# Kernel optimization log

Measured on AMD Instinct MI355X. Metric: run time of the kernel, lower is better.

The kernel has to match this reference:

```python
import jax, jax.numpy as jnp
import numpy as np

MARGIN = 0.5
SCALE = 64.0

N, D, C, S = 512, 512, 100000, 1


def setup_inputs() -> dict:
    key = jax.random.key(0)
    k1, k2, k3 = jax.random.split(key, 3)
    emb = jax.random.normal(k1, (N, D), dtype=jnp.float32)
    # Real face pipelines feed L2-normalized embeddings; also keeps acos well-conditioned.
    emb = emb / jnp.linalg.norm(emb, axis=1, keepdims=True)
    w = jax.random.normal(k2, (D, C, S), dtype=jnp.float32)
    labels = jax.random.randint(k3, (N,), 0, C)
    target = jax.nn.one_hot(labels, C, dtype=jnp.float32)  # [N, C]
    return {"embedding_batch": emb, "w_param": w, "target_batch": target}


def reference(embedding_batch, w_param, target_batch):
    # normalize class centers over the embedding dim (dim=0 of w)
    w_n = w_param / jnp.linalg.norm(w_param, axis=0, keepdims=True)  # [D, C, S]
    # cosine similarities via GEMM instead of broadcast mult-reduce: [N, C, S]
    cos = jnp.einsum('nd,dcs->ncs', embedding_batch, w_n)
    cos = jnp.clip(cos, -1.0, 1.0)
    cos = jnp.max(cos, axis=2)                    # best subclass -> [N, C]
    theta = jnp.arccos(cos)                       # [N, C]
    logits = jnp.cos(theta + target_batch * MARGIN) * SCALE
    # faithful to the original: softmax over dim=0 (the batch axis)
    return jax.nn.softmax(logits, axis=0)
```

## Files before the change

### kernel.cpp

```cpp
#include <hip/hip_runtime.h>
#include <hip/hip_bf16.h>


static constexpr int DIM    = 512;
static constexpr int NROWS  = 512;
static constexpr int NCLS   = 100000;
static constexpr int BC     = 32;
static constexpr int BK     = 32;
static constexpr int NSTEP  = DIM / BK;
static constexpr int MT     = NROWS / 16;
static constexpr int NBLK   = NCLS / BC;

static constexpr float COS_M = 0.87758256189037271611f;
static constexpr float SIN_M = 0.47942553860420300027f;
static constexpr float SCALE = 64.0f;

typedef __attribute__((ext_vector_type(8))) short bf16x8;
typedef __attribute__((ext_vector_type(4))) float f32x4;

#define SYNC_LDS()                                             \
  do {                                                         \
    asm volatile("s_waitcnt lgkmcnt(0)" ::: "memory");         \
    __builtin_amdgcn_s_barrier();                              \
    __builtin_amdgcn_sched_barrier(0);                         \
  } while (0)

__device__ __forceinline__ unsigned short f2bf(float f) {
  union { float f; unsigned u; } v; v.f = f;
  unsigned u = v.u;
  return (unsigned short)((u + 0x7FFFu + ((u >> 16) & 1u)) >> 16);
}

__global__ void prep_afrag(const float* __restrict__ emb,
                           unsigned short* __restrict__ afrag) {
  const int idx = blockIdx.x * blockDim.x + threadIdx.x;
  const int l  = idx & 63;
  const int mt = (idx >> 6) & 31;
  const int ks = idx >> 11;
  const int row = mt * 16 + (l & 15);
  const int k0  = ks * 32 + (l >> 4) * 8;

  unsigned short t[8];
#pragma unroll
  for (int j = 0; j < 8; ++j) t[j] = f2bf(emb[row * DIM + k0 + j]);

  uint4 v;
  v.x = (unsigned)t[0] | ((unsigned)t[1] << 16);
  v.y = (unsigned)t[2] | ((unsigned)t[3] << 16);
  v.z = (unsigned)t[4] | ((unsigned)t[5] << 16);
  v.w = (unsigned)t[6] | ((unsigned)t[7] << 16);
  *reinterpret_cast<uint4*>(&afrag[(size_t)idx * 8]) = v;
}

__device__ __forceinline__ float2 ldr2(const float* __restrict__ m, int r, int c) {
  return *reinterpret_cast<const float2*>(m + (size_t)r * NCLS + c);
}

__global__ __launch_bounds__(512, 4)
void arcface_fused(const float* __restrict__ w,
                   const float* __restrict__ tgt,
                   const unsigned short* __restrict__ afrag,
                   float* __restrict__ out) {
  __shared__ float S1[BK][36];
  __shared__ alignas(16) unsigned short S2[128][8];
  __shared__ float red[8][BC];
  __shared__ float colv[BC];
  __shared__ float rnS[BC];
  __shared__ unsigned char labL[NROWS];

  const int tid = threadIdx.x;
  const int wv  = tid >> 6;
  const int l   = tid & 63;
  const int lh  = l >> 4;
  const int ll  = l & 15;
  const int c0  = blockIdx.x * BC;

  const int sk  = tid >> 4;
  const int sc2 = tid & 15;
  const int scg = c0 + sc2 * 2;

  if (tid < 128) *reinterpret_cast<unsigned*>(&labL[tid * 4]) = 0u;
  __syncthreads();

  int cj[2];
#pragma unroll
  for (int j = 0; j < 2; ++j) cj[j] = c0 + j * 16 + ll;

  const unsigned short* pA[4];
#pragma unroll
  for (int i = 0; i < 4; ++i)
    pA[i] = afrag + ((size_t)(wv * 4 + i) * 64 + l) * 8;

  f32x4 acc[4][2] = {};
  float nx = 0.f, ny = 0.f;

  bf16x8 a[4], an[4];
#pragma unroll
  for (int i = 0; i < 4; ++i) {
    a[i]  = *reinterpret_cast<const bf16x8*>(pA[i]);
    an[i] = a[i];
  }
  float2 v0 = ldr2(w,   sk,      scg);
  float2 t0 = ldr2(tgt, sk,      scg);
  float2 v1 = ldr2(w,   BK + sk, scg);
  float2 t1 = ldr2(tgt, BK + sk, scg);

  for (int ks = 0; ks < NSTEP; ++ks) {
    nx += v0.x * v0.x; ny += v0.y * v0.y;
    *reinterpret_cast<float2*>(&S1[sk][sc2 * 2]) = v0;

    {
      const int row = ks * BK + sk;
      if (t0.x > 0.5f) labL[row] = (unsigned char)(sc2 * 2 + 1);
      if (t0.y > 0.5f) labL[row] = (unsigned char)(sc2 * 2 + 2);
    }
    v0 = v1; t0 = t1;

    if (ks + 1 < NSTEP) {
#pragma unroll
      for (int i = 0; i < 4; ++i)
        an[i] = *reinterpret_cast<const bf16x8*>(pA[i] + (size_t)(ks + 1) * MT * 64 * 8);
    }
    if (ks + 2 < NSTEP) {
      v1 = ldr2(w,   (ks + 2) * BK + sk, scg);
      t1 = ldr2(tgt, (ks + 2) * BK + sk, scg);
    }

    SYNC_LDS();

    if (tid < 256) {
      const int tc = tid & 31;
      const int tl = (tid >> 5) & 3;
      const int hf = (tid >> 7) & 1;
      const int kb = tl * 8 + hf * 4;
      float x0 = S1[kb + 0][tc], x1 = S1[kb + 1][tc];
      float x2 = S1[kb + 2][tc], x3 = S1[kb + 3][tc];
      uint2 pk;
      pk.x = (unsigned)f2bf(x0) | ((unsigned)f2bf(x1) << 16);
      pk.y = (unsigned)f2bf(x2) | ((unsigned)f2bf(x3) << 16);
      *reinterpret_cast<uint2*>(&S2[tl * 32 + tc][hf * 4]) = pk;
    }

    SYNC_LDS();

    bf16x8 b[2];
#pragma unroll
    for (int j = 0; j < 2; ++j)
      b[j] = *reinterpret_cast<const bf16x8*>(&S2[lh * 32 + j * 16 + ll][0]);
#pragma unroll
    for (int i = 0; i < 4; ++i)
#pragma unroll
      for (int j = 0; j < 2; ++j)
        acc[i][j] = __builtin_amdgcn_mfma_f32_16x16x32_bf16(a[i], b[j], acc[i][j], 0, 0, 0);
#pragma unroll
    for (int i = 0; i < 4; ++i) a[i] = an[i];
  }

  __syncthreads();
  *reinterpret_cast<float2*>(&S1[sk][sc2 * 2]) = make_float2(nx, ny);
  __syncthreads();
  if (tid < BC) {
    float s = 0.f;
#pragma unroll
    for (int k = 0; k < BK; ++k) s += S1[k][tid];
    rnS[tid] = rsqrtf(fmaxf(s, 1e-20f));
  }
  __syncthreads();
  float rn[2];
#pragma unroll
  for (int j = 0; j < 2; ++j) rn[j] = rnS[j * 16 + ll];

  int lab[4][4];
#pragma unroll
  for (int i = 0; i < 4; ++i)
#pragma unroll
    for (int q = 0; q < 4; ++q)
      lab[i][q] = (int)labL[wv * 64 + i * 16 + lh * 4 + q] - 1;

  float mx[2] = {-3.4e38f, -3.4e38f};
#pragma unroll
  for (int j = 0; j < 2; ++j) {
    const int jl = j * 16 + ll;
#pragma unroll
    for (int i = 0; i < 4; ++i) {
#pragma unroll
      for (int q = 0; q < 4; ++q) {
        float cosv = acc[i][j][q] * rn[j];
        cosv = fminf(fmaxf(cosv, -1.f), 1.f);
        float lg;
        if (lab[i][q] == jl) {
          const float s = sqrtf(fmaxf(1.f - cosv * cosv, 0.f));
          lg = cosv * COS_M - s * SIN_M;
        } else {
          lg = cosv;
        }
        lg *= SCALE;
        acc[i][j][q] = lg;
        mx[j] = fmaxf(mx[j], lg);
      }
    }
  }

#pragma unroll
  for (int j = 0; j < 2; ++j) {
    mx[j] = fmaxf(mx[j], __shfl_xor(mx[j], 16, 64));
    mx[j] = fmaxf(mx[j], __shfl_xor(mx[j], 32, 64));
  }
  if (l < 16) {
#pragma unroll
    for (int j = 0; j < 2; ++j) red[wv][j * 16 + l] = mx[j];
  }
  __syncthreads();
  if (tid < BC) {
    float m = red[0][tid];
#pragma unroll
    for (int v2 = 1; v2 < 8; ++v2) m = fmaxf(m, red[v2][tid]);
    colv[tid] = m;
  }
  __syncthreads();
  float cmax[2];
#pragma unroll
  for (int j = 0; j < 2; ++j) cmax[j] = colv[j * 16 + ll];

  float sme[2] = {0.f, 0.f};
#pragma unroll
  for (int j = 0; j < 2; ++j)
#pragma unroll
    for (int i = 0; i < 4; ++i)
#pragma unroll
      for (int q = 0; q < 4; ++q) {
        const float e = __expf(acc[i][j][q] - cmax[j]);
        acc[i][j][q] = e;
        sme[j] += e;
      }
#pragma unroll
  for (int j = 0; j < 2; ++j) {
    sme[j] += __shfl_xor(sme[j], 16, 64);
    sme[j] += __shfl_xor(sme[j], 32, 64);
  }
  __syncthreads();
  if (l < 16) {
#pragma unroll
    for (int j = 0; j < 2; ++j) red[wv][j * 16 + l] = sme[j];
  }
  __syncthreads();
  if (tid < BC) {
    float s = 0.f;
#pragma unroll
    for (int v2 = 0; v2 < 8; ++v2) s += red[v2][tid];
    colv[tid] = s;
  }
  __syncthreads();

  float rs[2];
#pragma unroll
  for (int j = 0; j < 2; ++j) rs[j] = 1.0f / colv[j * 16 + ll];

#pragma unroll
  for (int j = 0; j < 2; ++j) {
#pragma unroll
    for (int i = 0; i < 4; ++i) {
#pragma unroll
      for (int q = 0; q < 4; ++q) {
        const int row = wv * 64 + i * 16 + lh * 4 + q;
        out[(size_t)row * NCLS + cj[j]] = acc[i][j][q] * rs[j];
      }
    }
  }
}

extern "C" void kernel_launch(void* const* d_in, const int* in_sizes, int n_in,
                              void* d_out, int out_size, void* d_ws, size_t ws_size,
                              hipStream_t stream) {
  const float* emb = (const float*)d_in[0];
  const float* w   = (const float*)d_in[1];
  const float* tgt = (const float*)d_in[2];
  float* out = (float*)d_out;

  char* ws = (char*)d_ws;
  unsigned short* afrag = (unsigned short*)(ws + 4096);

  prep_afrag<<<64, 512, 0, stream>>>(emb, afrag);
  arcface_fused<<<NBLK, 512, 0, stream>>>(w, tgt, afrag, out);
}
```

Measured before the change: 231.1 us.

## Stage W tiles via async global_load_lds triple buffer and split warp roles

Replaces the register-staged W loads with direct global-to-LDS async loads into a three-deep LDS ring, and double-buffers the bf16 B tile so each k-step needs one barrier instead of two. Waves 0-3 convert W and compute norms while waves 4-7 scan the one-hot target with float4 loads. The loop is fully unrolled with hand-tuned vmcnt waits and raised priority around the MFMAs. The aim is to hide HBM latency and cut synchronisation. It relies on fragile hand-counted waitcnt values and leaves wave roles unevenly loaded.

Measured after the change: 225.7 us. -2.4%, faster.

```diff
diff --git a/kernel.cpp b/kernel.cpp
--- a/kernel.cpp
+++ b/kernel.cpp
@@ -18,12 +18,7 @@
 typedef __attribute__((ext_vector_type(8))) short bf16x8;
 typedef __attribute__((ext_vector_type(4))) float f32x4;
 
-#define SYNC_LDS()                                             \
-  do {                                                         \
-    asm volatile("s_waitcnt lgkmcnt(0)" ::: "memory");         \
-    __builtin_amdgcn_s_barrier();                              \
-    __builtin_amdgcn_sched_barrier(0);                         \
-  } while (0)
+#define MFMA16(A, B, C) __builtin_amdgcn_mfma_f32_16x16x32_bf16((A), (B), (C), 0, 0, 0)
 
 __device__ __forceinline__ unsigned short f2bf(float f) {
   union { float f; unsigned u; } v; v.f = f;
@@ -52,8 +47,16 @@
   *reinterpret_cast<uint4*>(&afrag[(size_t)idx * 8]) = v;
 }
 
-__device__ __forceinline__ float2 ldr2(const float* __restrict__ m, int r, int c) {
-  return *reinterpret_cast<const float2*>(m + (size_t)r * NCLS + c);
+__device__ __forceinline__ void stage_tile(const float* __restrict__ w, int c0,
+                                           int ks, int wv, int l,
+                                           char* s1base, int buf) {
+  const float* g = w + (size_t)(ks * BK + wv * 8 + (l >> 3)) * NCLS
+                     + (c0 + (l & 7) * 4);
+  const int off = __builtin_amdgcn_readfirstlane(buf * 4096 + wv * 1024);
+  __builtin_amdgcn_global_load_lds(
+      (const __attribute__((address_space(1))) void*)g,
+      (__attribute__((address_space(3))) void*)(s1base + off),
+      16, 0, 0);
 }
 
 __global__ __launch_bounds__(512, 4)
@@ -61,8 +64,9 @@
                    const float* __restrict__ tgt,
                    const unsigned short* __restrict__ afrag,
                    float* __restrict__ out) {
-  __shared__ float S1[BK][36];
-  __shared__ alignas(16) unsigned short S2[128][8];
+  __shared__ float S1[3][BK][BC];
+  __shared__ alignas(16) unsigned short S2[2][128][8];
+  __shared__ float nrmP[8][BC];
   __shared__ float red[8][BC];
   __shared__ float colv[BC];
   __shared__ float rnS[BC];
@@ -75,16 +79,14 @@
   const int ll  = l & 15;
   const int c0  = blockIdx.x * BC;
 
-  const int sk  = tid >> 4;
-  const int sc2 = tid & 15;
-  const int scg = c0 + sc2 * 2;
-
-  if (tid < 128) *reinterpret_cast<unsigned*>(&labL[tid * 4]) = 0u;
-  __syncthreads();
-
-  int cj[2];
-#pragma unroll
-  for (int j = 0; j < 2; ++j) cj[j] = c0 + j * 16 + ll;
+  const int tc = tid & 31;
+  const int tq = (tid >> 5) & 7;
+  const int tid2 = tid & 255;
+  const int tr   = tid2 >> 3;
+  const int tcc  = (tid2 & 7) * 4;
+
+  if (tid < 128) reinterpret_cast<unsigned*>(labL)[tid] = 0u;
+  __syncthreads();
 
   const unsigned short* pA[4];
 #pragma unroll
@@ -92,77 +94,103 @@
     pA[i] = afrag + ((size_t)(wv * 4 + i) * 64 + l) * 8;
 
   f32x4 acc[4][2] = {};
-  float nx = 0.f, ny = 0.f;
-
-  bf16x8 a[4], an[4];
-#pragma unroll
-  for (int i = 0; i < 4; ++i) {
-    a[i]  = *reinterpret_cast<const bf16x8*>(pA[i]);
-    an[i] = a[i];
-  }
-  float2 v0 = ldr2(w,   sk,      scg);
-  float2 t0 = ldr2(tgt, sk,      scg);
-  float2 v1 = ldr2(w,   BK + sk, scg);
-  float2 t1 = ldr2(tgt, BK + sk, scg);
-
-  for (int ks = 0; ks < NSTEP; ++ks) {
-    nx += v0.x * v0.x; ny += v0.y * v0.y;
-    *reinterpret_cast<float2*>(&S1[sk][sc2 * 2]) = v0;
-
-    {
-      const int row = ks * BK + sk;
-      if (t0.x > 0.5f) labL[row] = (unsigned char)(sc2 * 2 + 1);
-      if (t0.y > 0.5f) labL[row] = (unsigned char)(sc2 * 2 + 2);
-    }
-    v0 = v1; t0 = t1;
-
-    if (ks + 1 < NSTEP) {
-#pragma unroll
-      for (int i = 0; i < 4; ++i)
-        an[i] = *reinterpret_cast<const bf16x8*>(pA[i] + (size_t)(ks + 1) * MT * 64 * 8);
-    }
-    if (ks + 2 < NSTEP) {
-      v1 = ldr2(w,   (ks + 2) * BK + sk, scg);
-      t1 = ldr2(tgt, (ks + 2) * BK + sk, scg);
-    }
-
-    SYNC_LDS();
-
-    if (tid < 256) {
-      const int tc = tid & 31;
-      const int tl = (tid >> 5) & 3;
-      const int hf = (tid >> 7) & 1;
-      const int kb = tl * 8 + hf * 4;
-      float x0 = S1[kb + 0][tc], x1 = S1[kb + 1][tc];
-      float x2 = S1[kb + 2][tc], x3 = S1[kb + 3][tc];
-      uint2 pk;
-      pk.x = (unsigned)f2bf(x0) | ((unsigned)f2bf(x1) << 16);
-      pk.y = (unsigned)f2bf(x2) | ((unsigned)f2bf(x3) << 16);
-      *reinterpret_cast<uint2*>(&S2[tl * 32 + tc][hf * 4]) = pk;
-    }
-
-    SYNC_LDS();
-
-    bf16x8 b[2];
-#pragma unroll
-    for (int j = 0; j < 2; ++j)
-      b[j] = *reinterpret_cast<const bf16x8*>(&S2[lh * 32 + j * 16 + ll][0]);
-#pragma unroll
-    for (int i = 0; i < 4; ++i)
-#pragma unroll
-      for (int j = 0; j < 2; ++j)
-        acc[i][j] = __builtin_amdgcn_mfma_f32_16x16x32_bf16(a[i], b[j], acc[i][j], 0, 0, 0);
-#pragma unroll
-    for (int i = 0; i < 4; ++i) a[i] = an[i];
-  }
-
-  __syncthreads();
-  *reinterpret_cast<float2*>(&S1[sk][sc2 * 2]) = make_float2(nx, ny);
+  float nrm = 0.f;
+  bf16x8 areg[2][4];
+  float4 treg[2];
+  char* s1base = (char*)&S1[0][0][0];
+
+  if (wv < 4) {
+    stage_tile(w, c0, 0, wv, l, s1base, 0);
+    stage_tile(w, c0, 1, wv, l, s1base, 1);
+  }
+  __builtin_amdgcn_sched_barrier(0);
+#pragma unroll
+  for (int i = 0; i < 4; ++i)
+    areg[0][i] = *reinterpret_cast<const bf16x8*>(pA[i]);
+  __builtin_amdgcn_sched_barrier(0);
+  if (wv >= 4) {
+    treg[0] = *reinterpret_cast<const float4*>(tgt + (size_t)(0 * BK + tr) * NCLS + c0 + tcc);
+    treg[1] = *reinterpret_cast<const float4*>(tgt + (size_t)(1 * BK + tr) * NCLS + c0 + tcc);
+  }
+
+#define STEP(KS, VM)                                                            \
+  {                                                                             \
+    if (wv < 4) {                                                               \
+      asm volatile("s_waitcnt vmcnt(" #VM ")" ::: "memory");                    \
+      __builtin_amdgcn_sched_barrier(0);                                        \
+      if ((KS) + 2 < NSTEP)                                                     \
+        stage_tile(w, c0, (KS) + 2, wv, l, s1base, ((KS) + 2) % 3);             \
+      __builtin_amdgcn_sched_barrier(0);                                        \
+      const float x0 = S1[(KS) % 3][tq * 4 + 0][tc];                            \
+      const float x1 = S1[(KS) % 3][tq * 4 + 1][tc];                            \
+      const float x2 = S1[(KS) % 3][tq * 4 + 2][tc];                            \
+      const float x3 = S1[(KS) % 3][tq * 4 + 3][tc];                            \
+      nrm += x0 * x0 + x1 * x1 + x2 * x2 + x3 * x3;                             \
+      uint2 pk2;                                                                \
+      pk2.x = (unsigned)f2bf(x0) | ((unsigned)f2bf(x1) << 16);                  \
+      pk2.y = (unsigned)f2bf(x2) | ((unsigned)f2bf(x3) << 16);                  \
+      *reinterpret_cast<uint2*>(&S2[(KS) & 1][(tq >> 1) * 32 + tc][(tq & 1) * 4]) = pk2; \
+    } else {                                                                    \
+      const float4 tv = treg[(KS) & 1];                                         \
+      const int trow = (KS) * BK + tr;                                          \
+      if (tv.x > 0.5f) labL[trow] = (unsigned char)(tcc + 1);                   \
+      if (tv.y > 0.5f) labL[trow] = (unsigned char)(tcc + 2);                   \
+      if (tv.z > 0.5f) labL[trow] = (unsigned char)(tcc + 3);                   \
+      if (tv.w > 0.5f) labL[trow] = (unsigned char)(tcc + 4);                   \
+      if ((KS) + 2 < NSTEP)                                                     \
+        treg[(KS) & 1] = *reinterpret_cast<const float4*>(                      \
+            tgt + (size_t)(((KS) + 2) * BK + tr) * NCLS + c0 + tcc);            \
+    }                                                                           \
+    asm volatile("s_waitcnt lgkmcnt(0)" ::: "memory");                          \
+    __builtin_amdgcn_s_barrier();                                               \
+    __builtin_amdgcn_sched_barrier(0);                                          \
+    if ((KS) + 1 < NSTEP) {                                                     \
+      areg[((KS) + 1) & 1][0] = *reinterpret_cast<const bf16x8*>(pA[0] + (size_t)((KS) + 1) * MT * 64 * 8); \
+      areg[((KS) + 1) & 1][1] = *reinterpret_cast<const bf16x8*>(pA[1] + (size_t)((KS) + 1) * MT * 64 * 8); \
+      areg[((KS) + 1) & 1][2] = *reinterpret_cast<const bf16x8*>(pA[2] + (size_t)((KS) + 1) * MT * 64 * 8); \
+      areg[((KS) + 1) & 1][3] = *reinterpret_cast<const bf16x8*>(pA[3] + (size_t)((KS) + 1) * MT * 64 * 8); \
+    }                                                                           \
+    __builtin_amdgcn_sched_barrier(0);                                          \
+    __builtin_amdgcn_s_setprio(1);                                              \
+    {                                                                           \
+      const bf16x8 b0 = *reinterpret_cast<const bf16x8*>(&S2[(KS) & 1][lh * 32 + ll][0]);      \
+      const bf16x8 b1 = *reinterpret_cast<const bf16x8*>(&S2[(KS) & 1][lh * 32 + 16 + ll][0]); \
+      acc[0][0] = MFMA16(areg[(KS) & 1][0], b0, acc[0][0]);                     \
+      acc[0][1] = MFMA16(areg[(KS) & 1][0], b1, acc[0][1]);                     \
+      acc[1][0] = MFMA16(areg[(KS) & 1][1], b0, acc[1][0]);                     \
+      acc[1][1] = MFMA16(areg[(KS) & 1][1], b1, acc[1][1]);                     \
+      acc[2][0] = MFMA16(areg[(KS) & 1][2], b0, acc[2][0]);                     \
+      acc[2][1] = MFMA16(areg[(KS) & 1][2], b1, acc[2][1]);                     \
+      acc[3][0] = MFMA16(areg[(KS) & 1][3], b0, acc[3][0]);                     \
+      acc[3][1] = MFMA16(areg[(KS) & 1][3], b1, acc[3][1]);                     \
+    }                                                                           \
+    __builtin_amdgcn_s_setprio(0);                                              \
+  }
+
+  STEP(0, 5)
+  STEP(1, 9)
+  STEP(2, 9)
+  STEP(3, 9)
+  STEP(4, 9)
+  STEP(5, 9)
+  STEP(6, 9)
+  STEP(7, 9)
+  STEP(8, 9)
+  STEP(9, 9)
+  STEP(10, 9)
+  STEP(11, 9)
+  STEP(12, 9)
+  STEP(13, 9)
+  STEP(14, 9)
+  STEP(15, 8)
+#undef STEP
+
+  if (tid < 256) nrmP[tq][tc] = nrm;
   __syncthreads();
   if (tid < BC) {
     float s = 0.f;
 #pragma unroll
-    for (int k = 0; k < BK; ++k) s += S1[k][tid];
+    for (int t = 0; t < 8; ++t) s += nrmP[t][tid];
     rnS[tid] = rsqrtf(fmaxf(s, 1e-20f));
   }
   __syncthreads();
@@ -258,12 +286,13 @@
 
 #pragma unroll
   for (int j = 0; j < 2; ++j) {
+    const int cj = c0 + j * 16 + ll;
 #pragma unroll
     for (int i = 0; i < 4; ++i) {
 #pragma unroll
       for (int q = 0; q < 4; ++q) {
         const int row = wv * 64 + i * 16 + lh * 4 + q;
-        out[(size_t)row * NCLS + cj[j]] = acc[i][j][q] * rs[j];
+        out[(size_t)row * NCLS + cj] = acc[i][j][q] * rs[j];
       }
     }
   }
```

## Split W preprocessing into separate bf16 fragment kernel and barrier-free main GEMM

Applied to the files above, without the earlier changes.

Adds a kernel that reads W once, computes the per-class inverse norms and writes W as pre-swizzled bf16 MFMA fragments to workspace. The main kernel then loads B fragments straight from global memory, with no per-step LDS transpose or barriers, and reads the target labels with float4 loads. This trades an extra pass (write plus read of 100 MB of bf16 W) for less synchronisation and conversion work inside the GEMM loop.

Result: slower. 283.5 us (+22.7%).

```diff
diff --git a/kernel.cpp b/kernel.cpp
--- a/kernel.cpp
+++ b/kernel.cpp
@@ -18,12 +18,7 @@
 typedef __attribute__((ext_vector_type(8))) short bf16x8;
 typedef __attribute__((ext_vector_type(4))) float f32x4;
 
-#define SYNC_LDS()                                             \
-  do {                                                         \
-    asm volatile("s_waitcnt lgkmcnt(0)" ::: "memory");         \
-    __builtin_amdgcn_s_barrier();                              \
-    __builtin_amdgcn_sched_barrier(0);                         \
-  } while (0)
+#define MFMA16(A, B, C) __builtin_amdgcn_mfma_f32_16x16x32_bf16((A), (B), (C), 0, 0, 0)
 
 __device__ __forceinline__ unsigned short f2bf(float f) {
   union { float f; unsigned u; } v; v.f = f;
@@ -52,20 +47,67 @@
   *reinterpret_cast<uint4*>(&afrag[(size_t)idx * 8]) = v;
 }
 
-__device__ __forceinline__ float2 ldr2(const float* __restrict__ m, int r, int c) {
-  return *reinterpret_cast<const float2*>(m + (size_t)r * NCLS + c);
+__global__ __launch_bounds__(256)
+void wt_kernel(const float* __restrict__ w,
+               unsigned short* __restrict__ bfrag,
+               float* __restrict__ rnorm) {
+  __shared__ float S[32][33];
+  __shared__ float NRM[32][32];
+
+  const int t  = threadIdx.x;
+  const int cb = blockIdx.x;
+  const int c0 = cb * 32;
+
+  const int rk = t >> 3;
+  const int rc = (t & 7) * 4;
+
+  float4 nrm4 = {0.f, 0.f, 0.f, 0.f};
+
+  for (int p = 0; p < NSTEP; ++p) {
+    const float4 v = *reinterpret_cast<const float4*>(
+        w + (size_t)(p * BK + rk) * NCLS + c0 + rc);
+    nrm4.x += v.x * v.x; nrm4.y += v.y * v.y;
+    nrm4.z += v.z * v.z; nrm4.w += v.w * v.w;
+    __syncthreads();
+    *reinterpret_cast<float4*>(&S[rk][rc]) = v;
+    __syncthreads();
+
+    if (t < 128) {
+      const int l2 = t & 63;
+      const int j  = t >> 6;
+      const int col = j * 16 + (l2 & 15);
+      const int kb  = (l2 >> 4) * 8;
+      uint4 pk;
+      pk.x = (unsigned)f2bf(S[kb + 0][col]) | ((unsigned)f2bf(S[kb + 1][col]) << 16);
+      pk.y = (unsigned)f2bf(S[kb + 2][col]) | ((unsigned)f2bf(S[kb + 3][col]) << 16);
+      pk.z = (unsigned)f2bf(S[kb + 4][col]) | ((unsigned)f2bf(S[kb + 5][col]) << 16);
+      pk.w = (unsigned)f2bf(S[kb + 6][col]) | ((unsigned)f2bf(S[kb + 7][col]) << 16);
+      *reinterpret_cast<uint4*>(
+          &bfrag[(((size_t)(cb * NSTEP + p) * 2 + j) * 64 + l2) * 8]) = pk;
+    }
+  }
+
+  NRM[rk][rc + 0] = nrm4.x;
+  NRM[rk][rc + 1] = nrm4.y;
+  NRM[rk][rc + 2] = nrm4.z;
+  NRM[rk][rc + 3] = nrm4.w;
+  __syncthreads();
+  if (t < 32) {
+    float s = 0.f;
+#pragma unroll
+    for (int g = 0; g < 32; ++g) s += NRM[g][t];
+    rnorm[c0 + t] = rsqrtf(fmaxf(s, 1e-20f));
+  }
 }
 
 __global__ __launch_bounds__(512, 4)
-void arcface_fused(const float* __restrict__ w,
-                   const float* __restrict__ tgt,
-                   const unsigned short* __restrict__ afrag,
-                   float* __restrict__ out) {
-  __shared__ float S1[BK][36];
-  __shared__ alignas(16) unsigned short S2[128][8];
+void arcface_main(const unsigned short* __restrict__ bfrag,
+                  const unsigned short* __restrict__ afrag,
+                  const float* __restrict__ rnorm,
+                  const float* __restrict__ tgt,
+                  float* __restrict__ out) {
   __shared__ float red[8][BC];
   __shared__ float colv[BC];
-  __shared__ float rnS[BC];
   __shared__ unsigned char labL[NROWS];
 
   const int tid = threadIdx.x;
@@ -75,100 +117,49 @@
   const int ll  = l & 15;
   const int c0  = blockIdx.x * BC;
 
-  const int sk  = tid >> 4;
-  const int sc2 = tid & 15;
-  const int scg = c0 + sc2 * 2;
-
-  if (tid < 128) *reinterpret_cast<unsigned*>(&labL[tid * 4]) = 0u;
-  __syncthreads();
-
-  int cj[2];
-#pragma unroll
-  for (int j = 0; j < 2; ++j) cj[j] = c0 + j * 16 + ll;
-
-  const unsigned short* pA[4];
-#pragma unroll
-  for (int i = 0; i < 4; ++i)
-    pA[i] = afrag + ((size_t)(wv * 4 + i) * 64 + l) * 8;
+  if (tid < 128) reinterpret_cast<unsigned*>(labL)[tid] = 0u;
+  __syncthreads();
+
+  const int trow0 = wv * 64 + (l >> 3) * 8;
+  const int tcc   = (l & 7) * 4;
+  const float* tgtp = tgt + (size_t)trow0 * NCLS + c0 + tcc;
+
+  const unsigned short* pA = afrag + ((size_t)(wv * 4) * 64 + l) * 8;
+  const unsigned short* pB = bfrag + ((size_t)(blockIdx.x * NSTEP) * 2 * 64 + l) * 8;
 
   f32x4 acc[4][2] = {};
-  float nx = 0.f, ny = 0.f;
-
-  bf16x8 a[4], an[4];
-#pragma unroll
-  for (int i = 0; i < 4; ++i) {
-    a[i]  = *reinterpret_cast<const bf16x8*>(pA[i]);
-    an[i] = a[i];
-  }
-  float2 v0 = ldr2(w,   sk,      scg);
-  float2 t0 = ldr2(tgt, sk,      scg);
-  float2 v1 = ldr2(w,   BK + sk, scg);
-  float2 t1 = ldr2(tgt, BK + sk, scg);
-
+
+#pragma unroll
   for (int ks = 0; ks < NSTEP; ++ks) {
-    nx += v0.x * v0.x; ny += v0.y * v0.y;
-    *reinterpret_cast<float2*>(&S1[sk][sc2 * 2]) = v0;
-
-    {
-      const int row = ks * BK + sk;
-      if (t0.x > 0.5f) labL[row] = (unsigned char)(sc2 * 2 + 1);
-      if (t0.y > 0.5f) labL[row] = (unsigned char)(sc2 * 2 + 2);
-    }
-    v0 = v1; t0 = t1;
-
-    if (ks + 1 < NSTEP) {
-#pragma unroll
-      for (int i = 0; i < 4; ++i)
-        an[i] = *reinterpret_cast<const bf16x8*>(pA[i] + (size_t)(ks + 1) * MT * 64 * 8);
-    }
-    if (ks + 2 < NSTEP) {
-      v1 = ldr2(w,   (ks + 2) * BK + sk, scg);
-      t1 = ldr2(tgt, (ks + 2) * BK + sk, scg);
-    }
-
-    SYNC_LDS();
-
-    if (tid < 256) {
-      const int tc = tid & 31;
-      const int tl = (tid >> 5) & 3;
-      const int hf = (tid >> 7) & 1;
-      const int kb = tl * 8 + hf * 4;
-      float x0 = S1[kb + 0][tc], x1 = S1[kb + 1][tc];
-      float x2 = S1[kb + 2][tc], x3 = S1[kb + 3][tc];
-      uint2 pk;
-      pk.x = (unsigned)f2bf(x0) | ((unsigned)f2bf(x1) << 16);
-      pk.y = (unsigned)f2bf(x2) | ((unsigned)f2bf(x3) << 16);
-      *reinterpret_cast<uint2*>(&S2[tl * 32 + tc][hf * 4]) = pk;
-    }
-
-    SYNC_LDS();
-
-    bf16x8 b[2];
-#pragma unroll
-    for (int j = 0; j < 2; ++j)
-      b[j] = *reinterpret_cast<const bf16x8*>(&S2[lh * 32 + j * 16 + ll][0]);
+    const bf16x8 b0 = *reinterpret_cast<const bf16x8*>(pB + (size_t)ks * 1024);
+    const bf16x8 b1 = *reinterpret_cast<const bf16x8*>(pB + (size_t)ks * 1024 + 512);
+    bf16x8 a[4];
 #pragma unroll
     for (int i = 0; i < 4; ++i)
-#pragma unroll
-      for (int j = 0; j < 2; ++j)
-        acc[i][j] = __builtin_amdgcn_mfma_f32_16x16x32_bf16(a[i], b[j], acc[i][j], 0, 0, 0);
-#pragma unroll
-    for (int i = 0; i < 4; ++i) a[i] = an[i];
-  }
-
-  __syncthreads();
-  *reinterpret_cast<float2*>(&S1[sk][sc2 * 2]) = make_float2(nx, ny);
-  __syncthreads();
-  if (tid < BC) {
-    float s = 0.f;
-#pragma unroll
-    for (int k = 0; k < BK; ++k) s += S1[k][tid];
-    rnS[tid] = rsqrtf(fmaxf(s, 1e-20f));
-  }
-  __syncthreads();
+      a[i] = *reinterpret_cast<const bf16x8*>(pA + (size_t)(ks * MT + i) * 512);
+
+    if ((ks & 1) == 0) {
+      const int it = ks >> 1;
+      const float4 tv = *reinterpret_cast<const float4*>(tgtp + (size_t)it * NCLS);
+      const int trow = trow0 + it;
+      if (tv.x > 0.5f) labL[trow] = (unsigned char)(tcc + 1);
+      if (tv.y > 0.5f) labL[trow] = (unsigned char)(tcc + 2);
+      if (tv.z > 0.5f) labL[trow] = (unsigned char)(tcc + 3);
+      if (tv.w > 0.5f) labL[trow] = (unsigned char)(tcc + 4);
+    }
+
+#pragma unroll
+    for (int i = 0; i < 4; ++i) {
+      acc[i][0] = MFMA16(a[i], b0, acc[i][0]);
+      acc[i][1] = MFMA16(a[i], b1, acc[i][1]);
+    }
+  }
+
   float rn[2];
 #pragma unroll
-  for (int j = 0; j < 2; ++j) rn[j] = rnS[j * 16 + ll];
+  for (int j = 0; j < 2; ++j) rn[j] = rnorm[c0 + j * 16 + ll];
+
+  __syncthreads();
 
   int lab[4][4];
 #pragma unroll
@@ -258,12 +249,13 @@
 
 #pragma unroll
   for (int j = 0; j < 2; ++j) {
+    const int cj = c0 + j * 16 + ll;
 #pragma unroll
     for (int i = 0; i < 4; ++i) {
 #pragma unroll
       for (int q = 0; q < 4; ++q) {
         const int row = wv * 64 + i * 16 + lh * 4 + q;
-        out[(size_t)row * NCLS + cj[j]] = acc[i][j][q] * rs[j];
+        out[(size_t)row * NCLS + cj] = acc[i][j][q] * rs[j];
       }
     }
   }
@@ -279,7 +271,10 @@
 
   char* ws = (char*)d_ws;
   unsigned short* afrag = (unsigned short*)(ws + 4096);
+  float* rnorm          = (float*)(ws + (1u << 20));
+  unsigned short* bfrag = (unsigned short*)(ws + (2u << 20));
 
   prep_afrag<<<64, 512, 0, stream>>>(emb, afrag);
-  arcface_fused<<<NBLK, 512, 0, stream>>>(w, tgt, afrag, out);
-}
+  wt_kernel<<<NBLK, 256, 0, stream>>>(w, bfrag, rnorm);
+  arcface_main<<<NBLK, 512, 0, stream>>>(bfrag, afrag, rnorm, tgt, out);
+}
```
